# Kernel tuning notes

Hardware: AMD Instinct MI355X
Metric: run time of the kernel (lower is better)

The kernel has to match this reference:

```python
import jax, jax.numpy as jnp
import numpy as np

N_NODES = 40000
N_EDGES = 640000
D_MODEL = 128
N_LAYERS = 2


def setup_inputs() -> dict:
    key = jax.random.key(0)
    k1, k2, k3 = jax.random.split(key, 3)
    x = jax.random.normal(k1, (N_NODES, D_MODEL), dtype=jnp.float32)
    # Glorot-ish scaled weights per layer
    W = jax.random.normal(k2, (N_LAYERS, D_MODEL, D_MODEL), dtype=jnp.float32) / np.sqrt(D_MODEL)
    b = jnp.zeros((N_LAYERS, D_MODEL), dtype=jnp.float32)
    edge_index = jax.random.randint(k3, (2, N_EDGES), 0, N_NODES, dtype=jnp.int64)
    return {"x": x, "W": W, "b": b, "edge_index": edge_index}


def reference(x, W, b, edge_index):
    """Stacked DGL-style GraphConv (norm='both') layers on a flattened batched graph.

    Per layer: h' = D_in^{-1/2} A D_out^{-1/2} (h W) + b
    implemented as gather(src) -> per-edge normalize -> segment_sum(dst).
    """
    src = edge_index[0]
    dst = edge_index[1]
    n = x.shape[0]
    ones = jnp.ones((src.shape[0],), dtype=x.dtype)
    deg_out = jax.ops.segment_sum(ones, src, num_segments=n)  # out-degree of src nodes
    deg_in = jax.ops.segment_sum(ones, dst, num_segments=n)   # in-degree of dst nodes
    # symmetric normalization per edge: 1/sqrt(d_out(u) * d_in(v)), clipped to avoid div0
    edge_norm = jax.lax.rsqrt(jnp.clip(deg_out[src] * deg_in[dst], 1.0, None))  # [E]

    h = x
    for l in range(W.shape[0]):
        m = h @ W[l]                                   # [N, d] dense transform
        msg = m[src] * edge_norm[:, None]              # [E, d] gather + scale
        h = jax.ops.segment_sum(msg, dst, num_segments=n) + b[l]  # [N, d] scatter-add
    return h
```

## Files before the change

kernel.cpp:

```cpp
#include <hip/hip_runtime.h>
#include <hip/hip_fp16.h>

#define D_MODEL 128
#define NREP 8
#define FC 32
#define WCB 8

__device__ __forceinline__ bool sniff_i64(const void* ei) {
    const long long* p64 = (const long long*)ei;
    bool f64 = true;
#pragma unroll
    for (int i = 0; i < 8; ++i) {
        long long v = p64[i];
        f64 = f64 && (v >= 0 && v < (1LL << 31));
    }
    return f64;
}

__device__ __forceinline__ void load_edge(const void* ei, int e, int nE, bool f64,
                                          int& s, int& d) {
    if (f64) {
        const long long* p64 = (const long long*)ei;
        s = (int)p64[e];
        d = (int)p64[(size_t)nE + e];
    } else {
        const int* p32 = (const int*)ei;
        s = p32[e];
        d = p32[(size_t)nE + e];
    }
}

__global__ __launch_bounds__(1024) void hist_wc_kernel(const void* __restrict__ ei,
                                                       unsigned int* __restrict__ Cpk,
                                                       const float* __restrict__ W,
                                                       const float* __restrict__ b,
                                                       float* __restrict__ wc,
                                                       int nE, int n) {
    if (blockIdx.x >= FC) {
        int gid = (blockIdx.x - FC) * 1024 + threadIdx.x;
        const float* W2 = W + 128 * 128;
        for (int g = gid; g < 129 * 128; g += WCB * 1024) {
            int r = g >> 7, j = g & 127;
            const float* lhs = (r < 128) ? (W + (size_t)r * 128) : b;
            float acc = 0.f;
#pragma unroll 4
            for (int k = 0; k < 128; ++k) acc = fmaf(lhs[k], W2[(size_t)k * 128 + j], acc);
            wc[g] = acc;
        }
        return;
    }
    extern __shared__ unsigned int h[];
    bool f64 = sniff_i64(ei);
    int chunk = blockIdx.x;
    for (int i = threadIdx.x; i < n; i += 1024) h[i] = 0;
    __syncthreads();
    int ech = (nE + FC - 1) / FC;
    int e0 = chunk * ech;
    int e1 = min(nE, e0 + ech);
    if (f64) {
        const long long* p64 = (const long long*)ei;
        for (int e = e0 + threadIdx.x; e < e1; e += 1024) {
            atomicAdd(&h[(int)p64[e]], 1u);
            atomicAdd(&h[(int)p64[(size_t)nE + e]], 0x10000u);
        }
    } else {
        const int* p32 = (const int*)ei;
        for (int e = e0 + threadIdx.x; e < e1; e += 1024) {
            atomicAdd(&h[p32[e]], 1u);
            atomicAdd(&h[p32[(size_t)nE + e]], 0x10000u);
        }
    }
    __syncthreads();
    unsigned int* C = Cpk + (size_t)chunk * n;
    for (int i = threadIdx.x; i < n; i += 1024) C[i] = h[i];
}

__global__ __launch_bounds__(1024) void scanA_xcvt_kernel(const unsigned int* __restrict__ Cpk,
                                                          const float* __restrict__ x,
                                                          float* __restrict__ a,
                                                          float* __restrict__ bfac,
                                                          float* __restrict__ ab,
                                                          int* __restrict__ deg_in,
                                                          int* __restrict__ part,
                                                          float2* __restrict__ xh, int n) {
    __shared__ int wsum[16];
    __shared__ float sh_a[1024];
    int tid = threadIdx.x;
    int i = blockIdx.x * 1024 + tid;
    int lane = tid & 63, wid = tid >> 6;
    int din = 0;
    float fa = 0.f;
    if (i < n) {
        int dout = 0;
#pragma unroll 8
        for (int c = 0; c < FC; ++c) {
            unsigned int w = Cpk[(size_t)c * n + i];
            dout += (int)(w & 0xFFFFu);
            din += (int)(w >> 16);
        }
        fa = rsqrtf((float)max(dout, 1));
        float fb = rsqrtf((float)max(din, 1));
        a[i] = fa;
        bfac[i] = fb;
        ab[i] = fa * fb;
        deg_in[i] = din;
    }
    sh_a[tid] = fa;
    int v = din;
#pragma unroll
    for (int d = 32; d > 0; d >>= 1) v += __shfl_down(v, d, 64);
    if (lane == 0) wsum[wid] = v;
    __syncthreads();
    if (tid == 0) {
        int s = 0;
#pragma unroll
        for (int w = 0; w < 16; ++w) s += wsum[w];
        part[blockIdx.x] = s;
    }
    int rows_in_block = min(1024, n - blockIdx.x * 1024);
    if (rows_in_block <= 0) return;
    int total = rows_in_block * 32;
    const float4* xb = (const float4*)(x + (size_t)blockIdx.x * 1024 * D_MODEL);
    float2* xhb = xh + (size_t)blockIdx.x * 1024 * 32;
    for (int t = tid; t < total; t += 1024) {
        int rl = t >> 5;
        float s = sh_a[rl];
        float4 vv = xb[t];
        union { __half2 h2[2]; float2 f2; } u;
        u.h2[0] = __floats2half2_rn(s * vv.x, s * vv.y);
        u.h2[1] = __floats2half2_rn(s * vv.z, s * vv.w);
        xhb[t] = u.f2;
    }
}

__global__ __launch_bounds__(1024) void scanBC_kernel(const int* __restrict__ deg,
                                                      const int* __restrict__ part,
                                                      const unsigned int* __restrict__ Cpk,
                                                      int* __restrict__ offs,
                                                      int* __restrict__ base, int n) {
    __shared__ int wsum[16];
    __shared__ int blk_prefix;
    int tid = threadIdx.x;
    int i = blockIdx.x * 1024 + tid;
    int lane = tid & 63, wid = tid >> 6;
    if (tid == 0) {
        int acc = 0;
        for (int j = 0; j < (int)blockIdx.x; ++j) acc += part[j];
        blk_prefix = acc;
    }
    int v = (i < n) ? deg[i] : 0;
    int s = v;
#pragma unroll
    for (int d = 1; d < 64; d <<= 1) {
        int t = __shfl_up(s, d, 64);
        if (lane >= d) s += t;
    }
    if (lane == 63) wsum[wid] = s;
    __syncthreads();
    if (wid == 0) {
        int wsv = (lane < 16) ? wsum[lane] : 0;
#pragma unroll
        for (int d = 1; d < 16; d <<= 1) {
            int t = __shfl_up(wsv, d, 16);
            if ((lane & 15) >= d) wsv += t;
        }
        if (lane < 16) wsum[lane] = wsv;
    }
    __syncthreads();
    int pfx = blk_prefix + ((wid > 0) ? wsum[wid - 1] : 0);
    int incl = pfx + s;
    if (i < n) {
        int run = incl - v;
        offs[i] = run;
        if (i == n - 1) offs[n] = incl;
#pragma unroll 8
        for (int c = 0; c < FC; ++c) {
            base[(size_t)c * n + i] = run;
            run += (int)(Cpk[(size_t)c * n + i] >> 16);
        }
    }
}

__global__ __launch_bounds__(1024) void fill_lds_kernel(const void* __restrict__ ei,
                                                        const int* __restrict__ base,
                                                        int* __restrict__ csr_src,
                                                        int nE, int n) {
    extern __shared__ int cur[];
    bool f64 = sniff_i64(ei);
    int chunk = blockIdx.x;
    for (int i = threadIdx.x; i < n; i += 1024) cur[i] = base[(size_t)chunk * n + i];
    __syncthreads();
    int ech = (nE + FC - 1) / FC;
    int e0 = chunk * ech;
    int e1 = min(nE, e0 + ech);
    for (int e = e0 + threadIdx.x; e < e1; e += 1024) {
        int s, d;
        load_edge(ei, e, nE, f64, s, d);
        int slot = atomicAdd(&cur[d], 1);
        csr_src[slot] = s;
    }
}

__global__ __launch_bounds__(256) void agg0_kernel(const __half2* __restrict__ rows_in,
                                                   const int* __restrict__ offs,
                                                   const int* __restrict__ csr,
                                                   const float* __restrict__ ab,
                                                   __half2* __restrict__ out_rows, int n) {
    int node = blockIdx.x * 4 + (threadIdx.x >> 6);
    if (node >= n) return;
    node = __builtin_amdgcn_readfirstlane(node);
    int lane = threadIdx.x & 63;
    int beg = offs[node], end = offs[node + 1];
    float ax0 = 0.f, ay0 = 0.f, ax1 = 0.f, ay1 = 0.f;
    float ax2 = 0.f, ay2 = 0.f, ax3 = 0.f, ay3 = 0.f;
    int e = beg;
    for (; e + 3 < end; e += 4) {
        int s0 = csr[e], s1 = csr[e + 1], s2 = csr[e + 2], s3 = csr[e + 3];
        float2 f0 = __half22float2(rows_in[(size_t)s0 * 64 + lane]);
        float2 f1 = __half22float2(rows_in[(size_t)s1 * 64 + lane]);
        float2 f2 = __half22float2(rows_in[(size_t)s2 * 64 + lane]);
        float2 f3 = __half22float2(rows_in[(size_t)s3 * 64 + lane]);
        ax0 += f0.x; ay0 += f0.y;
        ax1 += f1.x; ay1 += f1.y;
        ax2 += f2.x; ay2 += f2.y;
        ax3 += f3.x; ay3 += f3.y;
    }
    for (; e < end; ++e) {
        int s0 = csr[e];
        float2 f0 = __half22float2(rows_in[(size_t)s0 * 64 + lane]);
        ax0 += f0.x; ay0 += f0.y;
    }
    float sx = (ax0 + ax1) + (ax2 + ax3);
    float sy = (ay0 + ay1) + (ay2 + ay3);
    float sc = ab[node];
    out_rows[(size_t)node * 64 + lane] = __floats2half2_rn(sc * sx, sc * sy);
}

__global__ __launch_bounds__(256, 4) void agg_gemm_kernel(const __half2* __restrict__ u,
                                                          const int* __restrict__ offs,
                                                          const int* __restrict__ csr,
                                                          const float* __restrict__ a_arr,
                                                          const float* __restrict__ bfac,
                                                          const float* __restrict__ wc,
                                                          const float* __restrict__ b2,
                                                          float* __restrict__ out, int n) {
    __shared__ float At[32][132];
    __shared__ float Ws[32][128];
    __shared__ float cS[32];
    int tid = threadIdx.x;
    int wv = tid >> 6, lane = tid & 63;
    int row0 = blockIdx.x * 32;

#pragma unroll 1
    for (int j = 0; j < 8; ++j) {
        int lr = wv * 8 + j;
        int node = row0 + lr;
        float sx = 0.f, sy = 0.f, cs = 0.f;
        if (node < n) {
            node = __builtin_amdgcn_readfirstlane(node);
            int beg = offs[node], end = offs[node + 1];
            float ax0 = 0.f, ay0 = 0.f, ax1 = 0.f, ay1 = 0.f;
            float ax2 = 0.f, ay2 = 0.f, ax3 = 0.f, ay3 = 0.f;
            int e = beg;
            for (; e + 3 < end; e += 4) {
                int s0 = csr[e], s1 = csr[e + 1], s2 = csr[e + 2], s3 = csr[e + 3];
                float2 f0 = __half22float2(u[(size_t)s0 * 64 + lane]);
                float2 f1 = __half22float2(u[(size_t)s1 * 64 + lane]);
                float2 f2 = __half22float2(u[(size_t)s2 * 64 + lane]);
                float2 f3 = __half22float2(u[(size_t)s3 * 64 + lane]);
                ax0 += f0.x; ay0 += f0.y;
                ax1 += f1.x; ay1 += f1.y;
                ax2 += f2.x; ay2 += f2.y;
                ax3 += f3.x; ay3 += f3.y;
                cs += (a_arr[s0] + a_arr[s1]) + (a_arr[s2] + a_arr[s3]);
            }
            for (; e < end; ++e) {
                int s0 = csr[e];
                float2 f0 = __half22float2(u[(size_t)s0 * 64 + lane]);
                ax0 += f0.x; ay0 += f0.y;
                cs += a_arr[s0];
            }
            sx = (ax0 + ax1) + (ax2 + ax3);
            sy = (ay0 + ay1) + (ay2 + ay3);
            if (lane == 0) cS[lr] = bfac[node] * cs;
        } else if (lane == 0) {
            cS[lr] = 0.f;
        }
        *(float2*)&At[lr][2 * lane] = make_float2(sx, sy);
    }

    int tc = tid & 31;
    int tr = tid >> 5;
    float acc[4][4] = {};
    for (int k0 = 0; k0 < D_MODEL; k0 += 32) {
        __syncthreads();
        {
            const float4* Wg = (const float4*)(wc + (size_t)k0 * D_MODEL);
            float4* WsV = (float4*)&Ws[0][0];
#pragma unroll
            for (int i = 0; i < 4; ++i) WsV[tid + 256 * i] = Wg[tid + 256 * i];
        }
        __syncthreads();
#pragma unroll
        for (int kk4 = 0; kk4 < 8; ++kk4) {
            float4 a4[4], w4[4];
#pragma unroll
            for (int i = 0; i < 4; ++i)
                a4[i] = *(const float4*)&At[4 * tr + i][k0 + 4 * kk4];
#pragma unroll
            for (int k = 0; k < 4; ++k)
                w4[k] = *(const float4*)&Ws[4 * kk4 + k][4 * tc];
#pragma unroll
            for (int i = 0; i < 4; ++i) {
                float av[4] = {a4[i].x, a4[i].y, a4[i].z, a4[i].w};
#pragma unroll
                for (int k = 0; k < 4; ++k) {
                    float wv4[4] = {w4[k].x, w4[k].y, w4[k].z, w4[k].w};
#pragma unroll
                    for (int j = 0; j < 4; ++j)
                        acc[i][j] = fmaf(av[k], wv4[j], acc[i][j]);
                }
            }
        }
    }
    float4 g4 = *(const float4*)(wc + 128 * 128 + 4 * tc);
    float4 b4 = *(const float4*)(b2 + 4 * tc);
#pragma unroll
    for (int i = 0; i < 4; ++i) {
        int row = row0 + 4 * tr + i;
        if (row < n) {
            float bf = bfac[row];
            float cv = cS[4 * tr + i];
            float4 o;
            o.x = bf * acc[i][0] + cv * g4.x + b4.x;
            o.y = bf * acc[i][1] + cv * g4.y + b4.y;
            o.z = bf * acc[i][2] + cv * g4.z + b4.z;
            o.w = bf * acc[i][3] + cv * g4.w + b4.w;
            *(float4*)(out + (size_t)row * D_MODEL + 4 * tc) = o;
        }
    }
}

__global__ void prep_kernel(const void* __restrict__ ei, int* __restrict__ rep_out,
                            int* __restrict__ rep_in, int nE, int n) {
    bool f64 = sniff_i64(ei);
    int e = blockIdx.x * blockDim.x + threadIdx.x;
    if (e >= nE) return;
    int s, d;
    load_edge(ei, e, nE, f64, s, d);
    int rep = blockIdx.x & (NREP - 1);
    atomicAdd(&rep_out[(size_t)rep * n + s], 1);
    atomicAdd(&rep_in[(size_t)rep * n + d], 1);
}

__global__ void deg_reduce_rep_kernel(const int* __restrict__ rep_out,
                                      const int* __restrict__ rep_in,
                                      float* __restrict__ a, float* __restrict__ bfac,
                                      float* __restrict__ ab, int* __restrict__ deg_in,
                                      int n) {
    int v = blockIdx.x * blockDim.x + threadIdx.x;
    if (v >= n) return;
    int dout = 0, din = 0;
#pragma unroll
    for (int r = 0; r < NREP; ++r) {
        dout += rep_out[(size_t)r * n + v];
        din += rep_in[(size_t)r * n + v];
    }
    float fa = rsqrtf((float)max(dout, 1));
    float fb = rsqrtf((float)max(din, 1));
    a[v] = fa;
    bfac[v] = fb;
    ab[v] = fa * fb;
    deg_in[v] = din;
}

__global__ __launch_bounds__(1024) void scanA_plain_kernel(const int* __restrict__ deg,
                                                           int* __restrict__ part, int n) {
    __shared__ int wsum[16];
    int i = blockIdx.x * 1024 + threadIdx.x;
    int lane = threadIdx.x & 63, wid = threadIdx.x >> 6;
    int v = (i < n) ? deg[i] : 0;
#pragma unroll
    for (int d = 32; d > 0; d >>= 1) v += __shfl_down(v, d, 64);
    if (lane == 0) wsum[wid] = v;
    __syncthreads();
    if (threadIdx.x == 0) {
        int s = 0;
#pragma unroll
        for (int w = 0; w < 16; ++w) s += wsum[w];
        part[blockIdx.x] = s;
    }
}

__global__ __launch_bounds__(1024) void scanC_plain_kernel(const int* __restrict__ deg,
                                                           const int* __restrict__ part,
                                                           int* __restrict__ offs, int n) {
    __shared__ int wsum[16];
    __shared__ int blk_prefix;
    int i = blockIdx.x * 1024 + threadIdx.x;
    int lane = threadIdx.x & 63, wid = threadIdx.x >> 6;
    if (threadIdx.x == 0) {
        int acc = 0;
        for (int j = 0; j < (int)blockIdx.x; ++j) acc += part[j];
        blk_prefix = acc;
    }
    int v = (i < n) ? deg[i] : 0;
    int s = v;
#pragma unroll
    for (int d = 1; d < 64; d <<= 1) {
        int t = __shfl_up(s, d, 64);
        if (lane >= d) s += t;
    }
    if (lane == 63) wsum[wid] = s;
    __syncthreads();
    if (wid == 0) {
        int wsv = (lane < 16) ? wsum[lane] : 0;
#pragma unroll
        for (int d = 1; d < 16; d <<= 1) {
            int t = __shfl_up(wsv, d, 16);
            if ((lane & 15) >= d) wsv += t;
        }
        if (lane < 16) wsum[lane] = wsv;
    }
    __syncthreads();
    int pfx = blk_prefix + ((wid > 0) ? wsum[wid - 1] : 0);
    int incl = pfx + s;
    if (i < n) {
        offs[i] = incl - v;
        if (i == n - 1) offs[n] = incl;
    }
}

__global__ void fill_kernel(const void* __restrict__ ei, const int* __restrict__ offs,
                            int* __restrict__ cursor, int* __restrict__ csr_src, int nE) {
    bool f64 = sniff_i64(ei);
    int e = blockIdx.x * blockDim.x + threadIdx.x;
    if (e >= nE) return;
    int s, d;
    load_edge(ei, e, nE, f64, s, d);
    int slot = offs[d] + atomicAdd(&cursor[d], 1);
    csr_src[slot] = s;
}

__global__ void xcvt_kernel(const float* __restrict__ x, const float* __restrict__ a,
                            float2* __restrict__ xh, int n4) {
    int idx = blockIdx.x * blockDim.x + threadIdx.x;
    if (idx >= n4) return;
    int row = idx >> 5;
    float s = a[row];
    float4 v = ((const float4*)x)[idx];
    union { __half2 h2[2]; float2 f2; } uu;
    uu.h2[0] = __floats2half2_rn(s * v.x, s * v.y);
    uu.h2[1] = __floats2half2_rn(s * v.z, s * v.w);
    xh[idx] = uu.f2;
}

__global__ void wc_plain_kernel(const float* __restrict__ W, const float* __restrict__ b,
                                float* __restrict__ wc) {
    int gid = blockIdx.x * blockDim.x + threadIdx.x;
    if (gid >= 129 * 128) return;
    int r = gid >> 7, j = gid & 127;
    const float* W2 = W + 128 * 128;
    const float* lhs = (r < 128) ? (W + (size_t)r * 128) : b;
    float acc = 0.f;
#pragma unroll 4
    for (int k = 0; k < 128; ++k) acc = fmaf(lhs[k], W2[(size_t)k * 128 + j], acc);
    wc[gid] = acc;
}

extern "C" void kernel_launch(void* const* d_in, const int* in_sizes, int n_in,
                              void* d_out, int out_size, void* d_ws, size_t ws_size,
                              hipStream_t stream) {
    const float* x = (const float*)d_in[0];
    const float* W = (const float*)d_in[1];
    const float* b = (const float*)d_in[2];
    const void* ei = d_in[3];
    const int D = D_MODEL;
    int N = in_sizes[0] / D;
    int E = in_sizes[3] / 2;
    float* out = (float*)d_out;

    char* p = (char*)d_ws;
    size_t off = 0;
    auto take = [&](size_t bytes) {
        void* r = p + off;
        off += (bytes + 255) & ~(size_t)255;
        return r;
    };
    __half2* xh   = (__half2*)take((size_t)N * D * 2);
    __half2* u    = (__half2*)take((size_t)N * D * 2);
    int* csr_src  = (int*)take((size_t)E * 4);
    float* a_arr  = (float*)take((size_t)N * 4);
    float* bfac   = (float*)take((size_t)N * 4);
    float* ab     = (float*)take((size_t)N * 4);
    int* deg_in   = (int*)take((size_t)N * 4);
    int* offs     = (int*)take((size_t)(N + 1) * 4);
    int* cursor   = (int*)take((size_t)N * 4);
    int* part     = (int*)take(256 * 4);
    float* wc     = (float*)take((size_t)129 * 128 * 4);
    unsigned int* Cpk = (unsigned int*)take((size_t)FC * N * 4);
    int* base     = (int*)take((size_t)FC * N * 4);
    size_t lds_need = off;

    size_t lds_bytes = (size_t)N * 4;
    bool use_lds = (lds_bytes <= 160000) && (lds_need <= ws_size);

    int eb = (E + 255) / 256;
    int G = (N + 1023) / 1024;

    if (use_lds) {
        hist_wc_kernel<<<FC + WCB, 1024, lds_bytes, stream>>>(ei, Cpk, W, b, wc, E, N);
        scanA_xcvt_kernel<<<G, 1024, 0, stream>>>(Cpk, x, a_arr, bfac, ab, deg_in,
                                                  part, (float2*)xh, N);
        scanBC_kernel<<<G, 1024, 0, stream>>>(deg_in, part, Cpk, offs, base, N);
        fill_lds_kernel<<<FC, 1024, lds_bytes, stream>>>(ei, base, csr_src, E, N);
    } else {
        int* rep_out = (int*)Cpk;
        int* rep_in  = (int*)base;
        if (lds_need > ws_size) {
            rep_out = (int*)u;
            rep_in  = (int*)((char*)u + (size_t)NREP * N * 4);
        }
        hipMemsetAsync(rep_out, 0, (size_t)NREP * N * 4, stream);
        hipMemsetAsync(rep_in, 0, (size_t)NREP * N * 4, stream);
        hipMemsetAsync(cursor, 0, (size_t)N * 4, stream);
        wc_plain_kernel<<<(129 * 128 + 255) / 256, 256, 0, stream>>>(W, b, wc);
        prep_kernel<<<eb, 256, 0, stream>>>(ei, rep_out, rep_in, E, N);
        deg_reduce_rep_kernel<<<(N + 255) / 256, 256, 0, stream>>>(rep_out, rep_in, a_arr,
                                                                   bfac, ab, deg_in, N);
        scanA_plain_kernel<<<G, 1024, 0, stream>>>(deg_in, part, N);
        scanC_plain_kernel<<<G, 1024, 0, stream>>>(deg_in, part, offs, N);
        fill_kernel<<<eb, 256, 0, stream>>>(ei, offs, cursor, csr_src, E);
        int n4 = N * (D / 4);
        xcvt_kernel<<<(n4 + 255) / 256, 256, 0, stream>>>(x, a_arr, (float2*)xh, n4);
    }

    agg0_kernel<<<(N + 3) / 4, 256, 0, stream>>>(xh, offs, csr_src, ab, u, N);
    agg_gemm_kernel<<<(N + 31) / 32, 256, 0, stream>>>(u, offs, csr_src, a_arr, bfac,
                                                       wc, b + 128, out, N);
}
```

Before: 177.5 us.

## Split fused second aggregation+GEMM into separate aggregation and GEMM kernels

Un-fuses the layer-2 aggregation from the GEMM: a templated aggregation kernel (one wavefront per node, gather loop unrolled by 8) writes fp16 aggregated rows and a per-node correction term to global memory, then a standalone tiled GEMM kernel reads them back with a transposed shared-memory A tile. The goal is better occupancy and latency hiding for the gather, which the fused kernel limited by giving each wave 8 sequential nodes. The cost is an extra kernel launch, an fp16 round trip of the aggregated matrix through global memory, and an extra rounding to half precision before the GEMM.

After: 149.1 us, median of 3. 16.0% less time.

```diff
diff --git a/kernel.cpp b/kernel.cpp
--- a/kernel.cpp
+++ b/kernel.cpp
@@ -201,97 +201,87 @@
     }
 }
 
-__global__ __launch_bounds__(256) void agg0_kernel(const __half2* __restrict__ rows_in,
-                                                   const int* __restrict__ offs,
-                                                   const int* __restrict__ csr,
-                                                   const float* __restrict__ ab,
-                                                   __half2* __restrict__ out_rows, int n) {
+template <int MODE>
+__global__ __launch_bounds__(256) void agg_kernel(const __half2* __restrict__ rows_in,
+                                                  const int* __restrict__ offs,
+                                                  const int* __restrict__ csr,
+                                                  const float* __restrict__ ab,
+                                                  const float* __restrict__ bfac,
+                                                  const float* __restrict__ a_arr,
+                                                  __half2* __restrict__ out_rows,
+                                                  float* __restrict__ c_out, int n) {
     int node = blockIdx.x * 4 + (threadIdx.x >> 6);
     if (node >= n) return;
     node = __builtin_amdgcn_readfirstlane(node);
     int lane = threadIdx.x & 63;
+    const __half2* rl = rows_in + lane;
     int beg = offs[node], end = offs[node + 1];
     float ax0 = 0.f, ay0 = 0.f, ax1 = 0.f, ay1 = 0.f;
     float ax2 = 0.f, ay2 = 0.f, ax3 = 0.f, ay3 = 0.f;
+    float cs = 0.f;
     int e = beg;
-    for (; e + 3 < end; e += 4) {
-        int s0 = csr[e], s1 = csr[e + 1], s2 = csr[e + 2], s3 = csr[e + 3];
-        float2 f0 = __half22float2(rows_in[(size_t)s0 * 64 + lane]);
-        float2 f1 = __half22float2(rows_in[(size_t)s1 * 64 + lane]);
-        float2 f2 = __half22float2(rows_in[(size_t)s2 * 64 + lane]);
-        float2 f3 = __half22float2(rows_in[(size_t)s3 * 64 + lane]);
+    for (; e + 7 < end; e += 8) {
+        int s0 = csr[e],     s1 = csr[e + 1], s2 = csr[e + 2], s3 = csr[e + 3];
+        int s4 = csr[e + 4], s5 = csr[e + 5], s6 = csr[e + 6], s7 = csr[e + 7];
+        __half2 v0 = rl[(size_t)s0 * 64];
+        __half2 v1 = rl[(size_t)s1 * 64];
+        __half2 v2 = rl[(size_t)s2 * 64];
+        __half2 v3 = rl[(size_t)s3 * 64];
+        __half2 v4 = rl[(size_t)s4 * 64];
+        __half2 v5 = rl[(size_t)s5 * 64];
+        __half2 v6 = rl[(size_t)s6 * 64];
+        __half2 v7 = rl[(size_t)s7 * 64];
+        float2 f0 = __half22float2(v0), f1 = __half22float2(v1);
+        float2 f2 = __half22float2(v2), f3 = __half22float2(v3);
+        float2 f4 = __half22float2(v4), f5 = __half22float2(v5);
+        float2 f6 = __half22float2(v6), f7 = __half22float2(v7);
+        ax0 += f0.x + f4.x; ay0 += f0.y + f4.y;
+        ax1 += f1.x + f5.x; ay1 += f1.y + f5.y;
+        ax2 += f2.x + f6.x; ay2 += f2.y + f6.y;
+        ax3 += f3.x + f7.x; ay3 += f3.y + f7.y;
+        if (MODE == 1)
+            cs += ((a_arr[s0] + a_arr[s1]) + (a_arr[s2] + a_arr[s3])) +
+                  ((a_arr[s4] + a_arr[s5]) + (a_arr[s6] + a_arr[s7]));
+    }
+    for (; e + 1 < end; e += 2) {
+        int s0 = csr[e], s1 = csr[e + 1];
+        float2 f0 = __half22float2(rl[(size_t)s0 * 64]);
+        float2 f1 = __half22float2(rl[(size_t)s1 * 64]);
         ax0 += f0.x; ay0 += f0.y;
         ax1 += f1.x; ay1 += f1.y;
-        ax2 += f2.x; ay2 += f2.y;
-        ax3 += f3.x; ay3 += f3.y;
-    }
-    for (; e < end; ++e) {
+        if (MODE == 1) cs += a_arr[s0] + a_arr[s1];
+    }
+    if (e < end) {
         int s0 = csr[e];
-        float2 f0 = __half22float2(rows_in[(size_t)s0 * 64 + lane]);
+        float2 f0 = __half22float2(rl[(size_t)s0 * 64]);
         ax0 += f0.x; ay0 += f0.y;
+        if (MODE == 1) cs += a_arr[s0];
     }
     float sx = (ax0 + ax1) + (ax2 + ax3);
     float sy = (ay0 + ay1) + (ay2 + ay3);
-    float sc = ab[node];
-    out_rows[(size_t)node * 64 + lane] = __floats2half2_rn(sc * sx, sc * sy);
-}
-
-__global__ __launch_bounds__(256, 4) void agg_gemm_kernel(const __half2* __restrict__ u,
-                                                          const int* __restrict__ offs,
-                                                          const int* __restrict__ csr,
-                                                          const float* __restrict__ a_arr,
-                                                          const float* __restrict__ bfac,
-                                                          const float* __restrict__ wc,
-                                                          const float* __restrict__ b2,
-                                                          float* __restrict__ out, int n) {
-    __shared__ float At[32][132];
+    if (MODE == 0) {
+        float sc = ab[node];
+        out_rows[(size_t)node * 64 + lane] = __floats2half2_rn(sc * sx, sc * sy);
+    } else {
+        out_rows[(size_t)node * 64 + lane] = __floats2half2_rn(sx, sy);
+        if (lane == 0) c_out[node] = bfac[node] * cs;
+    }
+}
+
+__global__ __launch_bounds__(256) void gemm_final_kernel(const __half2* __restrict__ A2,
+                                                         const float* __restrict__ wc,
+                                                         const float* __restrict__ bfac,
+                                                         const float* __restrict__ c_arr,
+                                                         const float* __restrict__ b2,
+                                                         float* __restrict__ out, int nRows) {
     __shared__ float Ws[32][128];
-    __shared__ float cS[32];
+    __shared__ float At[32][36];
     int tid = threadIdx.x;
-    int wv = tid >> 6, lane = tid & 63;
-    int row0 = blockIdx.x * 32;
-
-#pragma unroll 1
-    for (int j = 0; j < 8; ++j) {
-        int lr = wv * 8 + j;
-        int node = row0 + lr;
-        float sx = 0.f, sy = 0.f, cs = 0.f;
-        if (node < n) {
-            node = __builtin_amdgcn_readfirstlane(node);
-            int beg = offs[node], end = offs[node + 1];
-            float ax0 = 0.f, ay0 = 0.f, ax1 = 0.f, ay1 = 0.f;
-            float ax2 = 0.f, ay2 = 0.f, ax3 = 0.f, ay3 = 0.f;
-            int e = beg;
-            for (; e + 3 < end; e += 4) {
-                int s0 = csr[e], s1 = csr[e + 1], s2 = csr[e + 2], s3 = csr[e + 3];
-                float2 f0 = __half22float2(u[(size_t)s0 * 64 + lane]);
-                float2 f1 = __half22float2(u[(size_t)s1 * 64 + lane]);
-                float2 f2 = __half22float2(u[(size_t)s2 * 64 + lane]);
-                float2 f3 = __half22float2(u[(size_t)s3 * 64 + lane]);
-                ax0 += f0.x; ay0 += f0.y;
-                ax1 += f1.x; ay1 += f1.y;
-                ax2 += f2.x; ay2 += f2.y;
-                ax3 += f3.x; ay3 += f3.y;
-                cs += (a_arr[s0] + a_arr[s1]) + (a_arr[s2] + a_arr[s3]);
-            }
-            for (; e < end; ++e) {
-                int s0 = csr[e];
-                float2 f0 = __half22float2(u[(size_t)s0 * 64 + lane]);
-                ax0 += f0.x; ay0 += f0.y;
-                cs += a_arr[s0];
-            }
-            sx = (ax0 + ax1) + (ax2 + ax3);
-            sy = (ay0 + ay1) + (ay2 + ay3);
-            if (lane == 0) cS[lr] = bfac[node] * cs;
-        } else if (lane == 0) {
-            cS[lr] = 0.f;
-        }
-        *(float2*)&At[lr][2 * lane] = make_float2(sx, sy);
-    }
-
     int tc = tid & 31;
     int tr = tid >> 5;
+    int row0 = blockIdx.x * 32;
     float acc[4][4] = {};
+
     for (int k0 = 0; k0 < D_MODEL; k0 += 32) {
         __syncthreads();
         {
@@ -300,27 +290,31 @@
 #pragma unroll
             for (int i = 0; i < 4; ++i) WsV[tid + 256 * i] = Wg[tid + 256 * i];
         }
+        int k0h = k0 >> 1;
+#pragma unroll
+        for (int i = 0; i < 2; ++i) {
+            int lin = tid + 256 * i;
+            int r = lin >> 4;
+            int h = lin & 15;
+            int row = row0 + r;
+            __half2 v = (row < nRows) ? A2[(size_t)row * 64 + k0h + h]
+                                      : __floats2half2_rn(0.f, 0.f);
+            float2 f = __half22float2(v);
+            At[2 * h][r] = f.x;
+            At[2 * h + 1][r] = f.y;
+        }
         __syncthreads();
 #pragma unroll
-        for (int kk4 = 0; kk4 < 8; ++kk4) {
-            float4 a4[4], w4[4];
+        for (int kk = 0; kk < 32; ++kk) {
+            float4 w4 = *(const float4*)&Ws[kk][4 * tc];
+            float4 a4 = *(const float4*)&At[kk][4 * tr];
+            float wv[4] = {w4.x, w4.y, w4.z, w4.w};
+            float av[4] = {a4.x, a4.y, a4.z, a4.w};
 #pragma unroll
             for (int i = 0; i < 4; ++i)
-                a4[i] = *(const float4*)&At[4 * tr + i][k0 + 4 * kk4];
-#pragma unroll
-            for (int k = 0; k < 4; ++k)
-                w4[k] = *(const float4*)&Ws[4 * kk4 + k][4 * tc];
-#pragma unroll
-            for (int i = 0; i < 4; ++i) {
-                float av[4] = {a4[i].x, a4[i].y, a4[i].z, a4[i].w};
-#pragma unroll
-                for (int k = 0; k < 4; ++k) {
-                    float wv4[4] = {w4[k].x, w4[k].y, w4[k].z, w4[k].w};
-#pragma unroll
-                    for (int j = 0; j < 4; ++j)
-                        acc[i][j] = fmaf(av[k], wv4[j], acc[i][j]);
-                }
-            }
+#pragma unroll
+                for (int j = 0; j < 4; ++j)
+                    acc[i][j] = fmaf(av[i], wv[j], acc[i][j]);
         }
     }
     float4 g4 = *(const float4*)(wc + 128 * 128 + 4 * tc);
@@ -328,9 +322,9 @@
 #pragma unroll
     for (int i = 0; i < 4; ++i) {
         int row = row0 + 4 * tr + i;
-        if (row < n) {
+        if (row < nRows) {
             float bf = bfac[row];
-            float cv = cS[4 * tr + i];
+            float cv = c_arr[row];
             float4 o;
             o.x = bf * acc[i][0] + cv * g4.x + b4.x;
             o.y = bf * acc[i][1] + cv * g4.y + b4.y;
@@ -493,6 +487,7 @@
     float* a_arr  = (float*)take((size_t)N * 4);
     float* bfac   = (float*)take((size_t)N * 4);
     float* ab     = (float*)take((size_t)N * 4);
+    float* c_arr  = (float*)take((size_t)N * 4);
     int* deg_in   = (int*)take((size_t)N * 4);
     int* offs     = (int*)take((size_t)(N + 1) * 4);
     int* cursor   = (int*)take((size_t)N * 4);
@@ -501,6 +496,7 @@
     unsigned int* Cpk = (unsigned int*)take((size_t)FC * N * 4);
     int* base     = (int*)take((size_t)FC * N * 4);
     size_t lds_need = off;
+    __half2* t2 = xh;
 
     size_t lds_bytes = (size_t)N * 4;
     bool use_lds = (lds_bytes <= 160000) && (lds_need <= ws_size);
@@ -535,7 +531,10 @@
         xcvt_kernel<<<(n4 + 255) / 256, 256, 0, stream>>>(x, a_arr, (float2*)xh, n4);
     }
 
-    agg0_kernel<<<(N + 3) / 4, 256, 0, stream>>>(xh, offs, csr_src, ab, u, N);
-    agg_gemm_kernel<<<(N + 31) / 32, 256, 0, stream>>>(u, offs, csr_src, a_arr, bfac,
-                                                       wc, b + 128, out, N);
-}
+    agg_kernel<0><<<(N + 3) / 4, 256, 0, stream>>>(xh, offs, csr_src, ab, bfac, a_arr,
+                                                   u, c_arr, N);
+    agg_kernel<1><<<(N + 3) / 4, 256, 0, stream>>>(u, offs, csr_src, ab, bfac, a_arr,
+                                                   t2, c_arr, N);
+    gemm_final_kernel<<<(N + 31) / 32, 256, 0, stream>>>(t2, wc, bfac, c_arr,
+                                                         b + 128, out, N);
+}
```
